# Kernel optimization log

Measured on AMD Instinct MI355X. Metric: run time of the kernel, lower is better.

Reference implementation:

```python
import jax, jax.numpy as jnp
import numpy as np

NUM_HEADS = 16

def setup_inputs() -> dict:
    key = jax.random.key(0)
    k1, k2, k3 = jax.random.split(key, 3)
    B, S, D = 2, 2048, 1024
    return {
        "hidden_states": jax.random.normal(k1, (B, S, D), dtype=jnp.float32),
        "W_attn": jax.random.normal(k2, (D, 3 * D), dtype=jnp.float32) * 0.02,
        "b_attn": jnp.zeros((3 * D,), dtype=jnp.float32),
        "W_proj": jax.random.normal(k3, (D, D), dtype=jnp.float32) * 0.02,
        "b_proj": jnp.zeros((D,), dtype=jnp.float32),
    }

def reference(hidden_states, W_attn, b_attn, W_proj, b_proj):
    B, S, D = hidden_states.shape
    H = NUM_HEADS
    hd = D // H
    # qkv projection (Conv1D == addmm): [B,S,3D]
    qkv = hidden_states @ W_attn + b_attn
    q, k, v = jnp.split(qkv, 3, axis=-1)
    # split heads -> [B,H,S,hd]
    def split_heads(t):
        return t.reshape(B, S, H, hd).transpose(0, 2, 1, 3)
    q, k, v = split_heads(q), split_heads(k), split_heads(v)
    # scaled QK^T: [B,H,S,S]
    scores = jnp.einsum('bhqd,bhkd->bhqk', q, k) / jnp.asarray(hd ** 0.5, dtype=q.dtype)
    causal = jnp.tril(jnp.ones((S, S), dtype=bool))
    mask_value = jnp.finfo(scores.dtype).min
    scores = jnp.where(causal, scores, mask_value)
    probs = jax.nn.softmax(scores, axis=-1)  # attn_pdrop=0 -> no dropout
    out = jnp.einsum('bhqk,bhkd->bhqd', probs, v)
    # merge heads -> [B,S,D]
    out = out.transpose(0, 2, 1, 3).reshape(B, S, D)
    out = out @ W_proj + b_proj  # resid_pdrop=0 -> no dropout
    return out
```

## Files before the change

### kernel.cpp

```cpp
#include <hip/hip_runtime.h>
#include <math.h>

typedef __attribute__((ext_vector_type(8))) short bf16x8;
typedef __attribute__((ext_vector_type(4))) short bf16x4;
typedef __attribute__((ext_vector_type(4))) float f32x4;

#define MFMA16(a, b, c) __builtin_amdgcn_mfma_f32_16x16x32_bf16(a, b, c, 0, 0, 0)

#define GLOAD_LDS16(g, l)                                                        \
    __builtin_amdgcn_global_load_lds(                                            \
        (const __attribute__((address_space(1))) void*)(g),                      \
        (__attribute__((address_space(3))) void*)(l), 16, 0, 0)

#define SBAR() __builtin_amdgcn_s_barrier()
#define PRIO(x) __builtin_amdgcn_s_setprio(x)
#define VMW6 asm volatile("s_waitcnt vmcnt(6)" ::: "memory")
#define VMW4 asm volatile("s_waitcnt vmcnt(4)" ::: "memory")
#define VMW2 asm volatile("s_waitcnt vmcnt(2)" ::: "memory")
#define VMW0 asm volatile("s_waitcnt vmcnt(0)" ::: "memory")
#define NOPS ((void)0)

__device__ __forceinline__ short f2bf(float f) {
    union { float f; unsigned u; } x; x.f = f;
    unsigned r = (x.u + 0x7fffu + ((x.u >> 16) & 1u)) >> 16;
    return (short)r;
}

__global__ __launch_bounds__(256) void prep_kernel(
    const float* __restrict__ hs, short* __restrict__ hs_bf,
    const float* __restrict__ Wa, const float* __restrict__ Wp,
    short* __restrict__ WaT, short* __restrict__ WpT) {
    __shared__ float tile[32][33];
    const int bid = blockIdx.x;
    if (bid < 4096) {
        int i = bid * 256 + threadIdx.x;
        float4 v = ((const float4*)hs)[i];
        bf16x4 o;
        o[0] = f2bf(v.x); o[1] = f2bf(v.y); o[2] = f2bf(v.z); o[3] = f2bf(v.w);
        ((bf16x4*)hs_bf)[i] = o;
        return;
    }
    const int xb2 = bid - 4096;
    const int xbb = xb2 & 127;
    const int ky = xb2 >> 7;
    const float* W; short* Wt; int N, xb;
    if (xbb < 96) { W = Wa; Wt = WaT; N = 3072; xb = xbb; }
    else          { W = Wp; Wt = WpT; N = 1024; xb = xbb - 96; }
    const int K = 1024;
    int c = threadIdx.x & 31, r0 = threadIdx.x >> 5;
    int n0 = xb << 5, k0 = ky << 5;
#pragma unroll
    for (int i = 0; i < 4; i++) {
        int r = r0 + i * 8;
        tile[r][c] = W[(long)(k0 + r) * N + n0 + c];
    }
    __syncthreads();
#pragma unroll
    for (int i = 0; i < 4; i++) {
        int r = r0 + i * 8;
        Wt[(long)(n0 + r) * K + k0 + c] = f2bf(tile[c][r]);
    }
}

#define LDA8(IDX) (*(const bf16x8*)&ls[(IDX)])
#define SA(q, k1v, nbv) GLOAD_LDS16(Ags + (size_t)(q) * 65536 + (k1v), &ls[(nbv) + (q) * 4096 + swd])
#define SB(q, k1v, nbv) GLOAD_LDS16(Bgs + (size_t)(q) * 65536 + (k1v), &ls[(nbv) + 32768 + (q) * 4096 + swd])

#define PHASE_MFMA(M0_, M1_, aa0, ba0, aa1, ba1)              \
    PRIO(1);                                                  \
    acc[M0_][0] = MFMA16(aa0, b00, acc[M0_][0]);              \
    acc[M0_][1] = MFMA16(aa0, b10, acc[M0_][1]);              \
    acc[M0_][2] = MFMA16(aa0, b20, acc[M0_][2]);              \
    acc[M0_][3] = MFMA16(aa0, b30, acc[M0_][3]);              \
    acc[M1_][0] = MFMA16(ba0, b00, acc[M1_][0]);              \
    acc[M1_][1] = MFMA16(ba0, b10, acc[M1_][1]);              \
    acc[M1_][2] = MFMA16(ba0, b20, acc[M1_][2]);              \
    acc[M1_][3] = MFMA16(ba0, b30, acc[M1_][3]);              \
    acc[M0_][0] = MFMA16(aa1, b01, acc[M0_][0]);              \
    acc[M0_][1] = MFMA16(aa1, b11, acc[M0_][1]);              \
    acc[M0_][2] = MFMA16(aa1, b21, acc[M0_][2]);              \
    acc[M0_][3] = MFMA16(aa1, b31, acc[M0_][3]);              \
    acc[M1_][0] = MFMA16(ba1, b01, acc[M1_][0]);              \
    acc[M1_][1] = MFMA16(ba1, b11, acc[M1_][1]);              \
    acc[M1_][2] = MFMA16(ba1, b21, acc[M1_][2]);              \
    acc[M1_][3] = MFMA16(ba1, b31, acc[M1_][3]);              \
    PRIO(0);

#define KTILE(T, STG, VMP2, VMTAIL) do {                                              \
    const int cb = ((T) & 1) << 14;                                                   \
    const int nb = cb ^ 16384;                                                        \
    const int k1 = ((T) + 1) << 6;                                                    \
    (void)nb; (void)k1;                                                               \
                                                                    \
    if (STG) { SB(0, k1, nb); SB(1, k1, nb); }                                        \
    const bf16x8 b00 = LDA8(cb + 32768 + bro + sw0);                                  \
    const bf16x8 b01 = LDA8(cb + 32768 + bro + sw1);                                  \
    const bf16x8 b10 = LDA8(cb + 32768 + bro + 1024 + sw0);                           \
    const bf16x8 b11 = LDA8(cb + 32768 + bro + 1024 + sw1);                           \
    const bf16x8 b20 = LDA8(cb + 32768 + bro + 2048 + sw0);                           \
    const bf16x8 b21 = LDA8(cb + 32768 + bro + 2048 + sw1);                           \
    const bf16x8 b30 = LDA8(cb + 32768 + bro + 3072 + sw0);                           \
    const bf16x8 b31 = LDA8(cb + 32768 + bro + 3072 + sw1);                           \
    {                                                                                 \
        bf16x8 x0 = LDA8(cb + aro + sw0), x1 = LDA8(cb + aro + sw1);                  \
        bf16x8 y0 = LDA8(cb + aro + 1024 + sw0), y1 = LDA8(cb + aro + 1024 + sw1);    \
        SBAR();                                                                       \
        PHASE_MFMA(0, 1, x0, y0, x1, y1)                                              \
        SBAR();                                                                       \
    }                                                                                 \
                                                                    \
    if (STG) { SB(2, k1, nb); SB(3, k1, nb); }                                        \
    {                                                                                 \
        bf16x8 x0 = LDA8(cb + aro + 2048 + sw0), x1 = LDA8(cb + aro + 2048 + sw1);    \
        bf16x8 y0 = LDA8(cb + aro + 3072 + sw0), y1 = LDA8(cb + aro + 3072 + sw1);    \
        SBAR();                                                                       \
        PHASE_MFMA(2, 3, x0, y0, x1, y1)                                              \
        SBAR();                                                                       \
    }                                                                                 \
                                                                    \
    VMP2;                                                                             \
    SBAR();                                                                           \
    if (STG) { SA(0, k1, nb); SA(2, k1, nb); }                                        \
    {                                                                                 \
        bf16x8 x0 = LDA8(cb + aro + 4096 + sw0), x1 = LDA8(cb + aro + 4096 + sw1);    \
        bf16x8 y0 = LDA8(cb + aro + 5120 + sw0), y1 = LDA8(cb + aro + 5120 + sw1);    \
        PHASE_MFMA(4, 5, x0, y0, x1, y1)                                              \
        SBAR();                                                                       \
    }                                                                                 \
                                                                    \
    if (STG) { SA(1, k1, nb); SA(3, k1, nb); }                                        \
    {                                                                                 \
        bf16x8 x0 = LDA8(cb + aro + 6144 + sw0), x1 = LDA8(cb + aro + 6144 + sw1);    \
        bf16x8 y0 = LDA8(cb + aro + 7168 + sw0), y1 = LDA8(cb + aro + 7168 + sw1);    \
        SBAR();                                                                       \
        PHASE_MFMA(6, 7, x0, y0, x1, y1)                                              \
        VMTAIL;                                                                       \
        SBAR();                                                                       \
    }                                                                                 \
} while (0)

__global__ __launch_bounds__(512, 2) void gemm_qkv_kernel(
    const short* __restrict__ A, const short* __restrict__ Bt,
    const float* __restrict__ bias,
    short* __restrict__ QK, short* __restrict__ VTb) {
    __shared__ __align__(16) short ls[65536];
    const int tid = threadIdx.x;
    const int lane = tid & 63, l15 = lane & 15, quad = lane >> 4;
    const int w = tid >> 6, wm = w >> 2, wn = w & 3;
    const int m0 = blockIdx.y * 256, n0 = blockIdx.x * 256;
    const int e = l15 & 7;
    const int sgr = (w << 3) + (lane >> 3);
    const int sgc = ((lane & 7) ^ (lane >> 3)) << 3;
    const int swd = w << 9;
    const short* Ags = A + (size_t)(m0 + sgr) * 1024 + sgc;
    const short* Bgs = Bt + (size_t)(n0 + sgr) * 1024 + sgc;
    const int aro = (wm * 128 + l15) << 6;
    const int bro = (wn * 64 + l15) << 6;
    const int sw0 = (quad ^ e) << 3;
    const int sw1 = ((4 + quad) ^ e) << 3;

    f32x4 acc[8][4];
#pragma unroll
    for (int i = 0; i < 8; i++)
#pragma unroll
        for (int j = 0; j < 4; j++) acc[i][j] = (f32x4){0.f, 0.f, 0.f, 0.f};

    SB(0, 0, 0); SB(1, 0, 0); SB(2, 0, 0); SB(3, 0, 0);
    SA(0, 0, 0); SA(2, 0, 0); SA(1, 0, 0); SA(3, 0, 0);
    VMW2;
    SBAR();

#pragma unroll 2
    for (int t = 0; t < 14; ++t) { KTILE(t, 1, VMW4, VMW2); }
    KTILE(14, 1, VMW4, VMW0);
    KTILE(15, 0, VMW0, NOPS);

    __syncthreads();

    if (n0 < 2048) {
        const float scale = (n0 < 1024) ? 0.18033688011112042f : 1.0f;
#pragma unroll
        for (int nt = 0; nt < 4; nt++) {
            const int nn = n0 + wn * 64 + nt * 16 + l15;
            const float bv = bias[nn];
#pragma unroll
            for (int mt = 0; mt < 8; mt++)
#pragma unroll
                for (int r = 0; r < 4; r++) {
                    const int mm = m0 + wm * 128 + mt * 16 + quad * 4 + r;
                    QK[(long)mm * 2048 + nn] = f2bf((acc[mt][nt][r] + bv) * scale);
                }
        }
    } else {
        short* vt = &ls[w * 4352];
        const int hh = ((n0 - 2048) >> 6) + wn;
        const int bb = m0 >> 11;
        const int srow = (m0 & 2047) + wm * 128;
        const int sloc = (lane & 7) << 3;
#pragma unroll
        for (int half = 0; half < 2; half++) {
#pragma unroll
            for (int nt = 0; nt < 4; nt++) {
                const int nn = n0 + wn * 64 + nt * 16 + l15;
                const float bv = bias[nn];
                const int d_ = nt * 16 + l15;
#pragma unroll
                for (int mt = 0; mt < 4; mt++) {
                    const int mtg = half * 4 + mt;
                    bf16x4 pk;
#pragma unroll
                    for (int r = 0; r < 4; r++) pk[r] = f2bf(acc[mtg][nt][r] + bv);
                    *(bf16x4*)&vt[d_ * 68 + mt * 16 + quad * 4] = pk;
                }
            }
#pragma unroll
            for (int i = 0; i < 8; i++) {
                const int d = i * 8 + (lane >> 3);
                bf16x8 vv = *(const bf16x8*)&vt[d * 68 + sloc];
                *(bf16x8*)&VTb[((size_t)(bb * 16 + hh) * 64 + d) * 2048 + srow + half * 64 + sloc] = vv;
            }
        }
    }
}

#define PJ_ISSUE(K0, BB) do {                                                               \
    const int i0 = (w << 2);                                                                \
    GLOAD_LDS16(&Ap[(size_t)((i0 << 3) + lrow) * 1024 + (K0) + lgcol], &ls[(BB) + i0 * 512]);             \
    GLOAD_LDS16(&Ap[(size_t)(((i0 + 1) << 3) + lrow) * 1024 + (K0) + lgcol], &ls[(BB) + (i0 + 1) * 512]); \
    GLOAD_LDS16(&Ap[(size_t)(((i0 + 2) << 3) + lrow) * 1024 + (K0) + lgcol], &ls[(BB) + (i0 + 2) * 512]); \
    GLOAD_LDS16(&Ap[(size_t)(((i0 + 3) << 3) + lrow) * 1024 + (K0) + lgcol], &ls[(BB) + (i0 + 3) * 512]); \
    const int j0 = (w << 1);                                                                \
    GLOAD_LDS16(&Bp[(size_t)((j0 << 3) + lrow) * 1024 + (K0) + lgcol], &ls[(BB) + 8192 + j0 * 512]);      \
    GLOAD_LDS16(&Bp[(size_t)(((j0 + 1) << 3) + lrow) * 1024 + (K0) + lgcol], &ls[(BB) + 8192 + (j0 + 1) * 512]); \
} while (0)

__global__ __launch_bounds__(256, 2) void gemm_proj_kernel(
    const short* __restrict__ A, const short* __restrict__ Bt,
    const float* __restrict__ bias, float* __restrict__ outF) {
    __shared__ __align__(16) short ls[36864];
    const int tid = threadIdx.x;
    const int lane = tid & 63, l15 = lane & 15, quad = lane >> 4, w = tid >> 6;
    const int m0 = blockIdx.y * 128, n0 = blockIdx.x * 64;
    const int e = l15 & 7;
    const int lrow = lane >> 3;
    const int lgcol = ((lane & 7) ^ lrow) << 3;
    const short* Ap = A + (size_t)m0 * 1024;
    const short* Bp = Bt + (size_t)n0 * 1024;

    f32x4 acc[2][4];
#pragma unroll
    for (int i = 0; i < 2; i++)
#pragma unroll
        for (int j = 0; j < 4; j++) acc[i][j] = (f32x4){0.f, 0.f, 0.f, 0.f};

    PJ_ISSUE(0, 0);
    PJ_ISSUE(64, 12288);
    VMW6;
    SBAR();

    int cur = 0;
    for (int t = 0; t < 16; ++t) {
        const int bb = cur * 12288;
        if (t < 14) {
            const int nb2 = (cur == 0) ? 24576 : (cur - 1) * 12288;
            PJ_ISSUE((t + 2) << 6, nb2);
        }
#pragma unroll
        for (int kb = 0; kb < 8; kb += 4) {
            const int sw = (((kb + quad) ^ e) << 3);
            bf16x8 af0 = *(const bf16x8*)&ls[bb + (w * 32 + l15) * 64 + sw];
            bf16x8 af1 = *(const bf16x8*)&ls[bb + (w * 32 + 16 + l15) * 64 + sw];
            bf16x8 bf0 = *(const bf16x8*)&ls[bb + 8192 + (l15) * 64 + sw];
            bf16x8 bf1 = *(const bf16x8*)&ls[bb + 8192 + (16 + l15) * 64 + sw];
            bf16x8 bf2 = *(const bf16x8*)&ls[bb + 8192 + (32 + l15) * 64 + sw];
            bf16x8 bf3 = *(const bf16x8*)&ls[bb + 8192 + (48 + l15) * 64 + sw];
            PRIO(1);
            acc[0][0] = MFMA16(af0, bf0, acc[0][0]);
            acc[0][1] = MFMA16(af0, bf1, acc[0][1]);
            acc[0][2] = MFMA16(af0, bf2, acc[0][2]);
            acc[0][3] = MFMA16(af0, bf3, acc[0][3]);
            acc[1][0] = MFMA16(af1, bf0, acc[1][0]);
            acc[1][1] = MFMA16(af1, bf1, acc[1][1]);
            acc[1][2] = MFMA16(af1, bf2, acc[1][2]);
            acc[1][3] = MFMA16(af1, bf3, acc[1][3]);
            PRIO(0);
        }
        if (t < 14) { VMW6; SBAR(); }
        else if (t == 14) { VMW0; SBAR(); }
        cur = (cur == 2) ? 0 : cur + 1;
    }

#pragma unroll
    for (int nt = 0; nt < 4; nt++) {
        int nn = n0 + nt * 16 + l15;
        float bv = bias[nn];
#pragma unroll
        for (int mt = 0; mt < 2; mt++)
#pragma unroll
            for (int r = 0; r < 4; r++) {
                int mm = m0 + w * 32 + mt * 16 + quad * 4 + r;
                outF[(long)mm * 1024 + nn] = acc[mt][nt][r] + bv;
            }
    }
}

__global__ __launch_bounds__(256, 4) void attn_kernel(
    const short* __restrict__ QK, const short* __restrict__ VT,
    short* __restrict__ Ao) {
    __shared__ __align__(16) short Kt[2][64 * 64];
    __shared__ __align__(16) short Vt[2][64 * 64];
    __shared__ __align__(16) short Pt[4][1024];
    const int tid = threadIdx.x;
    const int lane = tid & 63, l15 = lane & 15, quad = lane >> 4, w = tid >> 6;
    const int bx = blockIdx.x;
    const int qt = 31 - (bx >> 5);
    const int hb = bx & 31;
    const int b = hb >> 4, h = hb & 15;
    const size_t rowbase = (size_t)b * 2048 * 2048 + h * 64;
    const short* Qb = QK + rowbase;
    const short* Kb = QK + rowbase + 1024;
    const short* Vh = VT + (size_t)hb * 64 * 2048;
    short* Pw = &Pt[w][0];
    const int e = l15 & 7;

    const int srow0 = tid >> 3;
    const int srow1 = srow0 + 32;
    const int sc4 = (tid & 7) ^ (srow0 & 7);
    const int wdst = w << 9;

    const long qr = (long)(qt * 64 + w * 16 + l15) * 2048;
    bf16x8 qf0 = *(const bf16x8*)&Qb[qr + quad * 8];
    bf16x8 qf1 = *(const bf16x8*)&Qb[qr + 32 + quad * 8];

    float l = 0.f;
    f32x4 o[4];
#pragma unroll
    for (int dt = 0; dt < 4; dt++) o[dt] = (f32x4){0.f, 0.f, 0.f, 0.f};

    const int nc = qt + 1;

    GLOAD_LDS16(&Kb[(size_t)srow0 * 2048 + sc4 * 8], &Kt[0][wdst]);
    GLOAD_LDS16(&Kb[(size_t)srow1 * 2048 + sc4 * 8], &Kt[0][2048 + wdst]);
    GLOAD_LDS16(&Vh[srow0 * 2048 + sc4 * 8], &Vt[0][wdst]);
    GLOAD_LDS16(&Vh[srow1 * 2048 + sc4 * 8], &Vt[0][2048 + wdst]);
    VMW0;
    SBAR();

    for (int c = 0; c < nc; c++) {
        const short* Kc = &Kt[c & 1][0];
        const short* Vc = &Vt[c & 1][0];
        if (c + 1 < nc) {
            const int k2 = (c + 1) * 64;
            const int nb = (c + 1) & 1;
            GLOAD_LDS16(&Kb[(size_t)(k2 + srow0) * 2048 + sc4 * 8], &Kt[nb][wdst]);
            GLOAD_LDS16(&Kb[(size_t)(k2 + srow1) * 2048 + sc4 * 8], &Kt[nb][2048 + wdst]);
            GLOAD_LDS16(&Vh[srow0 * 2048 + k2 + sc4 * 8], &Vt[nb][wdst]);
            GLOAD_LDS16(&Vh[srow1 * 2048 + k2 + sc4 * 8], &Vt[nb][2048 + wdst]);
        }

        f32x4 s[4];
#pragma unroll
        for (int t = 0; t < 4; t++) {
            bf16x8 k0f = *(const bf16x8*)&Kc[(t * 16 + l15) * 64 + ((quad ^ e) << 3)];
            bf16x8 k1f = *(const bf16x8*)&Kc[(t * 16 + l15) * 64 + (((4 + quad) ^ e) << 3)];
            f32x4 z = (f32x4){0.f, 0.f, 0.f, 0.f};
            z = MFMA16(k0f, qf0, z);
            z = MFMA16(k1f, qf1, z);
            s[t] = z;
        }

        if (c == nc - 1) {
#pragma unroll
            for (int t = 0; t < 4; t++)
#pragma unroll
                for (int r = 0; r < 4; r++)
                    if (t * 16 + quad * 4 + r > w * 16 + l15) s[t][r] = -INFINITY;
        }

#pragma unroll
        for (int t = 0; t < 4; t++) {
            bf16x4 pw;
#pragma unroll
            for (int r = 0; r < 4; r++) {
                float pv = __builtin_amdgcn_exp2f(s[t][r]);
                l += pv;
                pw[r] = f2bf(pv);
            }
            *(bf16x4*)&Pw[l15 * 64 + (((2 * t + (quad >> 1)) ^ e) << 3) + ((quad & 1) << 2)] = pw;
        }

        bf16x8 pf0 = *(const bf16x8*)&Pw[l15 * 64 + ((quad ^ e) << 3)];
        bf16x8 pf1 = *(const bf16x8*)&Pw[l15 * 64 + (((4 + quad) ^ e) << 3)];
#pragma unroll
        for (int dt = 0; dt < 4; dt++) {
            bf16x8 v0f = *(const bf16x8*)&Vc[(dt * 16 + l15) * 64 + ((quad ^ e) << 3)];
            bf16x8 v1f = *(const bf16x8*)&Vc[(dt * 16 + l15) * 64 + (((4 + quad) ^ e) << 3)];
            o[dt] = MFMA16(v0f, pf0, o[dt]);
            o[dt] = MFMA16(v1f, pf1, o[dt]);
        }

        VMW0;
        SBAR();
    }

    l += __shfl_xor(l, 16);
    l += __shfl_xor(l, 32);
    const float rl = 1.f / l;

    const int qs = qt * 64 + w * 16 + l15;
    const long base = ((long)(b * 2048 + qs)) * 1024 + h * 64;
#pragma unroll
    for (int dt = 0; dt < 4; dt++) {
        bf16x4 wv;
#pragma unroll
        for (int r = 0; r < 4; r++) wv[r] = f2bf(o[dt][r] * rl);
        *(bf16x4*)&Ao[base + dt * 16 + quad * 4] = wv;
    }
}

extern "C" void kernel_launch(void* const* d_in, const int* in_sizes, int n_in,
                              void* d_out, int out_size, void* d_ws, size_t ws_size,
                              hipStream_t stream) {
    const float* hs = (const float*)d_in[0];
    const float* W_attn = (const float*)d_in[1];
    const float* b_attn = (const float*)d_in[2];
    const float* W_proj = (const float*)d_in[3];
    const float* b_proj = (const float*)d_in[4];
    float* out = (float*)d_out;

    const size_t MB = 1024 * 1024;
    char* ws = (char*)d_ws;
    short* hs_bf = (short*)ws;
    short* attn_o = hs_bf;
    short* WaT = (short*)(ws + 8 * MB);
    short* WpT = (short*)(ws + 14 * MB);
    short* QK = (short*)(ws + 16 * MB);
    short* VTb = (short*)(ws + 32 * MB);

    prep_kernel<<<8192, 256, 0, stream>>>(hs, hs_bf, W_attn, W_proj, WaT, WpT);
    gemm_qkv_kernel<<<dim3(12, 16), 512, 0, stream>>>(hs_bf, WaT, b_attn, QK, VTb);
    attn_kernel<<<1024, 256, 0, stream>>>(QK, VTb, attn_o);
    gemm_proj_kernel<<<dim3(16, 32), 256, 0, stream>>>(attn_o, WpT, b_proj, out);
}
```

Baseline: 167.8 us.

## Stage Q/K epilogue through LDS for vector stores; compute row sums via MFMA

```diff
diff --git a/kernel.cpp b/kernel.cpp
--- a/kernel.cpp
+++ b/kernel.cpp
@@ -179,17 +179,32 @@
 
     if (n0 < 2048) {
         const float scale = (n0 < 1024) ? 0.18033688011112042f : 1.0f;
-#pragma unroll
-        for (int nt = 0; nt < 4; nt++) {
-            const int nn = n0 + wn * 64 + nt * 16 + l15;
-            const float bv = bias[nn];
-#pragma unroll
-            for (int mt = 0; mt < 8; mt++)
-#pragma unroll
-                for (int r = 0; r < 4; r++) {
-                    const int mm = m0 + wm * 128 + mt * 16 + quad * 4 + r;
-                    QK[(long)mm * 2048 + nn] = f2bf((acc[mt][nt][r] + bv) * scale);
+        short* qt_ = &ls[w * 4352];
+        const int colbase = n0 + wn * 64;
+        const int rrow = lane >> 3;
+        const int rcol = (lane & 7) << 3;
+#pragma unroll
+        for (int half = 0; half < 2; half++) {
+#pragma unroll
+            for (int nt = 0; nt < 4; nt++) {
+                const int nn = colbase + nt * 16 + l15;
+                const float bv = bias[nn];
+#pragma unroll
+                for (int mt = 0; mt < 4; mt++) {
+                    const int mtg = half * 4 + mt;
+#pragma unroll
+                    for (int r = 0; r < 4; r++)
+                        qt_[(mt * 16 + quad * 4 + r) * 68 + nt * 16 + l15] =
+                            f2bf((acc[mtg][nt][r] + bv) * scale);
                 }
+            }
+#pragma unroll
+            for (int i = 0; i < 8; i++) {
+                const int mrow = i * 8 + rrow;
+                bf16x8 vv = *(const bf16x8*)&qt_[mrow * 68 + rcol];
+                const int mm = m0 + wm * 128 + half * 64 + mrow;
+                *(bf16x8*)&QK[(size_t)mm * 2048 + colbase + rcol] = vv;
+            }
         }
     } else {
         short* vt = &ls[w * 4352];
@@ -324,7 +339,6 @@
     const int e = l15 & 7;
 
     const int srow0 = tid >> 3;
-    const int srow1 = srow0 + 32;
     const int sc4 = (tid & 7) ^ (srow0 & 7);
     const int wdst = w << 9;
 
@@ -332,17 +346,24 @@
     bf16x8 qf0 = *(const bf16x8*)&Qb[qr + quad * 8];
     bf16x8 qf1 = *(const bf16x8*)&Qb[qr + 32 + quad * 8];
 
-    float l = 0.f;
+    bf16x8 ones;
+#pragma unroll
+    for (int i = 0; i < 8; i++) ones[i] = (short)0x3F80;
+
+    f32x4 lacc = (f32x4){0.f, 0.f, 0.f, 0.f};
     f32x4 o[4];
 #pragma unroll
     for (int dt = 0; dt < 4; dt++) o[dt] = (f32x4){0.f, 0.f, 0.f, 0.f};
 
     const int nc = qt + 1;
 
-    GLOAD_LDS16(&Kb[(size_t)srow0 * 2048 + sc4 * 8], &Kt[0][wdst]);
-    GLOAD_LDS16(&Kb[(size_t)srow1 * 2048 + sc4 * 8], &Kt[0][2048 + wdst]);
-    GLOAD_LDS16(&Vh[srow0 * 2048 + sc4 * 8], &Vt[0][wdst]);
-    GLOAD_LDS16(&Vh[srow1 * 2048 + sc4 * 8], &Vt[0][2048 + wdst]);
+    const short* kp = Kb + (size_t)srow0 * 2048 + sc4 * 8;
+    const short* vp = Vh + (size_t)srow0 * 2048 + sc4 * 8;
+
+    GLOAD_LDS16(kp, &Kt[0][wdst]);
+    GLOAD_LDS16(kp + 32 * 2048, &Kt[0][2048 + wdst]);
+    GLOAD_LDS16(vp, &Vt[0][wdst]);
+    GLOAD_LDS16(vp + 32 * 2048, &Vt[0][2048 + wdst]);
     VMW0;
     SBAR();
 
@@ -350,12 +371,13 @@
         const short* Kc = &Kt[c & 1][0];
         const short* Vc = &Vt[c & 1][0];
         if (c + 1 < nc) {
-            const int k2 = (c + 1) * 64;
+            kp += 64 * 2048;
+            vp += 64;
             const int nb = (c + 1) & 1;
-            GLOAD_LDS16(&Kb[(size_t)(k2 + srow0) * 2048 + sc4 * 8], &Kt[nb][wdst]);
-            GLOAD_LDS16(&Kb[(size_t)(k2 + srow1) * 2048 + sc4 * 8], &Kt[nb][2048 + wdst]);
-            GLOAD_LDS16(&Vh[srow0 * 2048 + k2 + sc4 * 8], &Vt[nb][wdst]);
-            GLOAD_LDS16(&Vh[srow1 * 2048 + k2 + sc4 * 8], &Vt[nb][2048 + wdst]);
+            GLOAD_LDS16(kp, &Kt[nb][wdst]);
+            GLOAD_LDS16(kp + 32 * 2048, &Kt[nb][2048 + wdst]);
+            GLOAD_LDS16(vp, &Vt[nb][wdst]);
+            GLOAD_LDS16(vp + 32 * 2048, &Vt[nb][2048 + wdst]);
         }
 
         f32x4 s[4];
@@ -381,11 +403,8 @@
         for (int t = 0; t < 4; t++) {
             bf16x4 pw;
 #pragma unroll
-            for (int r = 0; r < 4; r++) {
-                float pv = __builtin_amdgcn_exp2f(s[t][r]);
-                l += pv;
-                pw[r] = f2bf(pv);
-            }
+            for (int r = 0; r < 4; r++)
+                pw[r] = f2bf(__builtin_amdgcn_exp2f(s[t][r]));
             *(bf16x4*)&Pw[l15 * 64 + (((2 * t + (quad >> 1)) ^ e) << 3) + ((quad & 1) << 2)] = pw;
         }
 
@@ -398,14 +417,14 @@
             o[dt] = MFMA16(v0f, pf0, o[dt]);
             o[dt] = MFMA16(v1f, pf1, o[dt]);
         }
+        lacc = MFMA16(ones, pf0, lacc);
+        lacc = MFMA16(ones, pf1, lacc);
 
         VMW0;
         SBAR();
     }
 
-    l += __shfl_xor(l, 16);
-    l += __shfl_xor(l, 32);
-    const float rl = 1.f / l;
+    const float rl = 1.f / lacc[0];
 
     const int qs = qt * 64 + w * 16 + l15;
     const long base = ((long)(b * 2048 + qs)) * 1024 + h * 64;
```

Measured after the change: 168.4 us. No clear change (+0.4%).
